# Kernel tuning notes

Measured on AMD Instinct MI355X. Metric: run time of the kernel, lower is better.

The kernel has to match this reference:

```python
import jax, jax.numpy as jnp
import numpy as np

B, C, N = 8, 256, 4096

def setup_inputs() -> dict:
    key = jax.random.key(0)
    k1, k2, k3 = jax.random.split(key, 3)
    pts_feat = jax.random.normal(k1, (B, C, N), dtype=jnp.float32)
    # Conv1d(channels, channels, 1, bias=False) weight is [C_out, C_in, 1] -> store as [C_out, C_in]
    scale = 1.0 / np.sqrt(C)
    Wq = jax.random.uniform(k2, (C, C), dtype=jnp.float32, minval=-scale, maxval=scale)
    Wk = jax.random.uniform(k3, (C, C), dtype=jnp.float32, minval=-scale, maxval=scale)
    return {"pts_feat": pts_feat, "Wq": Wq, "Wk": Wk}

def reference(pts_feat, Wq, Wk):
    # 1x1 conv == channel-wise matmul. x_q: [B, N, C], x_k: [B, C, N]
    x_q = jnp.einsum('bcn,dc->bnd', pts_feat, Wq)
    x_k = jnp.einsum('bcn,dc->bdn', pts_feat, Wk)
    logits = jnp.einsum('bnc,bcm->bnm', x_q, x_k)          # [B, N, N]
    attn = jax.nn.softmax(logits, axis=-1)
    attn = attn / (1e-8 + attn.sum(axis=-1, keepdims=True))
    # torch.einsum('bnn,bnc->bnc', attn, feat) takes the DIAGONAL of attn
    # and scales each point's raw feature vector by it (no contraction).
    diag = jnp.diagonal(attn, axis1=1, axis2=2)            # [B, N]
    x_attn = pts_feat * diag[:, None, :]                   # [B, C, N]
    return x_attn
```

## Files before the change

kernel.cpp:

```cpp
#include <hip/hip_runtime.h>
#include <hip/hip_bf16.h>
#include <cstdint>

#define B_ 8
#define C_ 256
#define N_ 4096

typedef __bf16 bf16;
typedef __bf16 bf16x8 __attribute__((ext_vector_type(8)));
typedef float f32x4 __attribute__((ext_vector_type(4)));
typedef unsigned int u32;

__device__ __forceinline__ void async_ld16(const void* g, void* l) {
  __builtin_amdgcn_global_load_lds(
      (const __attribute__((address_space(1))) void*)g,
      (__attribute__((address_space(3))) void*)l, 16, 0, 0);
}

__device__ __forceinline__ float bh2f(unsigned short u) {
  union { u32 i; float f; } x; x.i = ((u32)u) << 16; return x.f;
}
__device__ __forceinline__ unsigned short f2bh(float f) {
  union { float f; u32 i; } x; x.f = f;
  u32 i = x.i + 0x7fffu + ((x.i >> 16) & 1u);
  return (unsigned short)(i >> 16);
}

__device__ __forceinline__ bool wave_sniff_fp32(const unsigned short* p) {
  int l = threadIdx.x & 63;
  unsigned short u = p[2 * l];
  int e = (u >> 7) & 0xff;
  unsigned long long m = __ballot(e >= 112 && e <= 142);
  return __popcll(m) < 32;
}

__global__ __launch_bounds__(256) void k_wconv(const void* __restrict__ W0,
                                               const void* __restrict__ W1,
                                               unsigned short* __restrict__ Wc0,
                                               unsigned short* __restrict__ Wc1) {
  const void* Wv = blockIdx.y ? W1 : W0;
  unsigned short* Wc = blockIdx.y ? Wc1 : Wc0;
  bool f32 = wave_sniff_fp32((const unsigned short*)Wv);
  int i = (blockIdx.x * 256 + threadIdx.x) * 4;
  if (f32) {
    float4 v = *(const float4*)((const float*)Wv + i);
    unsigned short o0 = f2bh(v.x), o1 = f2bh(v.y), o2 = f2bh(v.z), o3 = f2bh(v.w);
    uint2 o; o.x = ((u32)o1 << 16) | o0; o.y = ((u32)o3 << 16) | o2;
    *(uint2*)(Wc + i) = o;
  } else {
    uint2 v = *(const uint2*)((const unsigned short*)Wv + i);
    *(uint2*)(Wc + i) = v;
  }
}

__global__ __launch_bounds__(256) void k_transpose(const void* __restrict__ Fv,
                                                   unsigned short* __restrict__ Ft) {
  bool f32 = wave_sniff_fp32((const unsigned short*)Fv);
  __shared__ unsigned short tile[64 * 66];
  int n0 = blockIdx.x * 64, c0 = blockIdx.y * 64, b = blockIdx.z;
  int t = threadIdx.x;
#pragma unroll
  for (int p = 0; p < 2; ++p) {
    int c = (t >> 3) + 32 * p;
    int n = (t & 7) * 8;
    size_t off = (size_t)(b * C_ + c0 + c) * N_ + n0 + n;
    unsigned short vals[8];
    if (f32) {
      const float* src = (const float*)Fv + off;
      float4 v0 = *(const float4*)(src);
      float4 v1 = *(const float4*)(src + 4);
      vals[0] = f2bh(v0.x); vals[1] = f2bh(v0.y); vals[2] = f2bh(v0.z); vals[3] = f2bh(v0.w);
      vals[4] = f2bh(v1.x); vals[5] = f2bh(v1.y); vals[6] = f2bh(v1.z); vals[7] = f2bh(v1.w);
    } else {
      uint4 v = *(const uint4*)((const unsigned short*)Fv + off);
      vals[0] = (unsigned short)(v.x & 0xffffu); vals[1] = (unsigned short)(v.x >> 16);
      vals[2] = (unsigned short)(v.y & 0xffffu); vals[3] = (unsigned short)(v.y >> 16);
      vals[4] = (unsigned short)(v.z & 0xffffu); vals[5] = (unsigned short)(v.z >> 16);
      vals[6] = (unsigned short)(v.w & 0xffffu); vals[7] = (unsigned short)(v.w >> 16);
    }
#pragma unroll
    for (int s = 0; s < 8; ++s) tile[c * 66 + n + s] = vals[s];
  }
  __syncthreads();
#pragma unroll
  for (int p = 0; p < 4; ++p) {
    int n = (t >> 4) + 16 * p;
    int cq = (t & 15) * 4;
    unsigned short e0 = tile[(cq + 0) * 66 + n];
    unsigned short e1 = tile[(cq + 1) * 66 + n];
    unsigned short e2 = tile[(cq + 2) * 66 + n];
    unsigned short e3 = tile[(cq + 3) * 66 + n];
    uint2 o;
    o.x = ((u32)e1 << 16) | e0;
    o.y = ((u32)e3 << 16) | e2;
    *(uint2*)(Ft + ((size_t)(b * N_ + n0 + n) * C_ + c0 + cq)) = o;
  }
}

__global__ __launch_bounds__(256) void k_proj(const bf16* __restrict__ Ft,
                                              const bf16* __restrict__ Wq,
                                              const bf16* __restrict__ Wk,
                                              bf16* __restrict__ Qt,
                                              bf16* __restrict__ Kt) {
  __shared__ bf16 As[128 * 32];
  __shared__ bf16 Bs[128 * 32];
  int n0 = blockIdx.x * 128;
  int b = blockIdx.y;
  int z = blockIdx.z;
  int d0 = (z & 1) * 128;
  const bf16* W = (z >> 1) ? Wk : Wq;
  bf16* Dst = (z >> 1) ? Kt : Qt;
  int t = threadIdx.x;
  int w = t >> 6, l = t & 63;
  int wm = (w & 1) * 64, wn = (w >> 1) * 64;
  int lr = l & 15, lq = l >> 4;
  const size_t fbase = (size_t)b * N_ * C_;

  f32x4 acc[4][4] = {};
  for (int kc = 0; kc < 8; ++kc) {
    __syncthreads();
#pragma unroll
    for (int r = 0; r < 2; ++r) {
      int ci = r * 4 + w;
      int e = ci * 64 + l;
      int row = e >> 2, coff = (e & 3) * 8;
      async_ld16(Ft + fbase + (size_t)(n0 + row) * C_ + kc * 32 + coff, As + ci * 512);
      async_ld16(W + (size_t)(d0 + row) * C_ + kc * 32 + coff, Bs + ci * 512);
    }
    __syncthreads();
    bf16x8 a[4], bb[4];
#pragma unroll
    for (int i = 0; i < 4; ++i)
      a[i] = *(const bf16x8*)(As + (wm + 16 * i + lr) * 32 + lq * 8);
#pragma unroll
    for (int j = 0; j < 4; ++j)
      bb[j] = *(const bf16x8*)(Bs + (wn + 16 * j + lr) * 32 + lq * 8);
#pragma unroll
    for (int i = 0; i < 4; ++i)
#pragma unroll
      for (int j = 0; j < 4; ++j)
        acc[i][j] = __builtin_amdgcn_mfma_f32_16x16x32_bf16(a[i], bb[j], acc[i][j], 0, 0, 0);
  }
#pragma unroll
  for (int i = 0; i < 4; ++i)
#pragma unroll
    for (int j = 0; j < 4; ++j)
#pragma unroll
      for (int r = 0; r < 4; ++r) {
        int row = n0 + wm + 16 * i + lq * 4 + r;
        int col = d0 + wn + 16 * j + lr;
        Dst[fbase + (size_t)row * C_ + col] = (bf16)acc[i][j][r];
      }
}

__global__ __launch_bounds__(256, 4) void k_attn(const bf16* __restrict__ Qt,
                                                 const bf16* __restrict__ Kt,
                                                 float* __restrict__ snn,
                                                 float* __restrict__ lsum) {
  __shared__ bf16 Ks[8 * 64 * 32];
  int bid = blockIdx.x;
  int b = bid & 7, h = (bid >> 3) & 1, ntile = bid >> 4;
  int n0 = ntile * 128;
  int t = threadIdx.x, w = t >> 6, l = t & 63;
  int lr = l & 15, lq = l >> 4;
  int wrow = w * 32;
  const size_t gbase = (size_t)b * N_ * C_;

  bf16x8 a[2][8];
#pragma unroll
  for (int i = 0; i < 2; ++i)
#pragma unroll
    for (int kc = 0; kc < 8; ++kc)
      a[i][kc] = *(const bf16x8*)(Qt + gbase + (size_t)(n0 + wrow + 16 * i + lr) * C_ + kc * 32 + lq * 8);

  float part[8];
#pragma unroll
  for (int s = 0; s < 8; ++s) part[s] = 0.f;

  int m_base = h * 2048;
  bool has_diag = ((ntile >> 4) == h);
  int d0 = (ntile & 15) * 2;

  int srow = t >> 2, scoff = (t & 3) * 8;

  for (int it = 0; it < 32; ++it) {
    int m0 = m_base + it * 64;
    __syncthreads();
#pragma unroll
    for (int kc = 0; kc < 8; ++kc)
      async_ld16(Kt + gbase + (size_t)(m0 + srow) * C_ + kc * 32 + scoff,
                 Ks + kc * 2048 + t * 8);
    __syncthreads();
    f32x4 acc[2][4] = {};
#pragma unroll
    for (int kc = 0; kc < 8; ++kc) {
      bf16x8 bb[4];
#pragma unroll
      for (int j = 0; j < 4; ++j)
        bb[j] = *(const bf16x8*)(Ks + kc * 2048 + (16 * j + lr) * 32 + lq * 8);
#pragma unroll
      for (int i = 0; i < 2; ++i)
#pragma unroll
        for (int j = 0; j < 4; ++j)
          acc[i][j] = __builtin_amdgcn_mfma_f32_16x16x32_bf16(a[i][kc], bb[j], acc[i][j], 0, 0, 0);
    }
    bool dit = has_diag && ((it >> 1) == (ntile & 15));
#pragma unroll
    for (int i = 0; i < 2; ++i)
#pragma unroll
      for (int j = 0; j < 4; ++j)
#pragma unroll
        for (int r = 0; r < 4; ++r) {
          float e = __expf(acc[i][j][r]);
          part[i * 4 + r] += e;
          if (dit) {
            int rloc = wrow + 16 * i + lq * 4 + r;
            int cloc = 16 * j + lr;
            if ((it - d0) * 64 + cloc == rloc) snn[b * N_ + n0 + rloc] = e;
          }
        }
  }

#pragma unroll
  for (int s = 0; s < 8; ++s) {
    float v = part[s];
    v += __shfl_xor(v, 1);
    v += __shfl_xor(v, 2);
    v += __shfl_xor(v, 4);
    v += __shfl_xor(v, 8);
    part[s] = v;
  }
  if (lr == 0) {
#pragma unroll
    for (int i = 0; i < 2; ++i)
#pragma unroll
      for (int r = 0; r < 4; ++r)
        lsum[((size_t)h * B_ + b) * N_ + n0 + wrow + 16 * i + lq * 4 + r] = part[i * 4 + r];
  }
}

__global__ __launch_bounds__(256) void k_scale(const void* __restrict__ Fv,
                                               const float* __restrict__ snn,
                                               const float* __restrict__ lsum,
                                               void* __restrict__ Outv) {
  bool f32 = wave_sniff_fp32((const unsigned short*)Fv);
  int g = blockIdx.x * 256 + threadIdx.x;
  size_t base = (size_t)g * 8;
  int n = (int)(base & (N_ - 1));
  int b = (int)(base >> 20);
  float4 s0 = *(const float4*)(snn + (size_t)b * N_ + n);
  float4 s1 = *(const float4*)(snn + (size_t)b * N_ + n + 4);
  float4 l00 = *(const float4*)(lsum + (size_t)b * N_ + n);
  float4 l01 = *(const float4*)(lsum + (size_t)b * N_ + n + 4);
  float4 l10 = *(const float4*)(lsum + (size_t)(B_ + b) * N_ + n);
  float4 l11 = *(const float4*)(lsum + (size_t)(B_ + b) * N_ + n + 4);
  const float c1 = 1.0f + 1e-8f;
  float dd[8];
  dd[0] = s0.x / ((l00.x + l10.x) * c1);
  dd[1] = s0.y / ((l00.y + l10.y) * c1);
  dd[2] = s0.z / ((l00.z + l10.z) * c1);
  dd[3] = s0.w / ((l00.w + l10.w) * c1);
  dd[4] = s1.x / ((l01.x + l11.x) * c1);
  dd[5] = s1.y / ((l01.y + l11.y) * c1);
  dd[6] = s1.z / ((l01.z + l11.z) * c1);
  dd[7] = s1.w / ((l01.w + l11.w) * c1);
  if (f32) {
    const float* F = (const float*)Fv + base;
    float* O = (float*)Outv + base;
    float4 a0 = *(const float4*)(F);
    float4 a1 = *(const float4*)(F + 4);
    float4 o0, o1;
    o0.x = a0.x * dd[0]; o0.y = a0.y * dd[1]; o0.z = a0.z * dd[2]; o0.w = a0.w * dd[3];
    o1.x = a1.x * dd[4]; o1.y = a1.y * dd[5]; o1.z = a1.z * dd[6]; o1.w = a1.w * dd[7];
    *(float4*)(O) = o0;
    *(float4*)(O + 4) = o1;
  } else {
    uint4 v = *(const uint4*)((const unsigned short*)Fv + base);
    u32 vv[4] = {v.x, v.y, v.z, v.w};
    u32 o[4];
#pragma unroll
    for (int k = 0; k < 4; ++k) {
      float lo = bh2f((unsigned short)(vv[k] & 0xffffu)) * dd[2 * k];
      float hi = bh2f((unsigned short)(vv[k] >> 16)) * dd[2 * k + 1];
      o[k] = ((u32)f2bh(hi) << 16) | f2bh(lo);
    }
    uint4 ov; ov.x = o[0]; ov.y = o[1]; ov.z = o[2]; ov.w = o[3];
    *(uint4*)((unsigned short*)Outv + base) = ov;
  }
}

extern "C" void kernel_launch(void* const* d_in, const int* in_sizes, int n_in,
                              void* d_out, int out_size, void* d_ws, size_t ws_size,
                              hipStream_t stream) {
  (void)in_sizes; (void)n_in; (void)out_size; (void)ws_size;
  const void* F = d_in[0];
  const void* Wq = d_in[1];
  const void* Wk = d_in[2];
  char* ws = (char*)d_ws;
  bf16* Ft = (bf16*)(ws);
  bf16* Qt = (bf16*)(ws + (16u << 20));
  bf16* Kt = (bf16*)(ws + (32u << 20));
  char* tail = ws + (48u << 20);
  float* snn = (float*)(tail);
  float* lsum = (float*)(tail + 131072);
  bf16* Wqc = (bf16*)(tail + 131072 + 262144);
  bf16* Wkc = (bf16*)(tail + 131072 + 262144 + 131072);

  k_wconv<<<dim3(64, 2), 256, 0, stream>>>(Wq, Wk, (unsigned short*)Wqc, (unsigned short*)Wkc);
  k_transpose<<<dim3(N_ / 64, C_ / 64, B_), 256, 0, stream>>>(F, (unsigned short*)Ft);
  k_proj<<<dim3(N_ / 128, B_, 4), 256, 0, stream>>>(Ft, Wqc, Wkc, Qt, Kt);
  k_attn<<<512, 256, 0, stream>>>(Qt, Kt, snn, lsum);
  k_scale<<<(B_ * C_ * N_ / 8) / 256, 256, 0, stream>>>(F, snn, lsum, d_out);
}
```

Baseline: 189.3 us.

## Fold Wq and Wk into one combined matrix, halve projections, split attention four ways

Logits are rewritten as F^T (Wq^T Wk) F. A small kernel computes the combined CxC matrix, so only one projection G = F^T M is produced, and the attention kernel multiplies G against the transposed features directly. This drops the separate K projection and its memory traffic. The attention key range is split four ways, giving 1024 blocks instead of 512. Shared-memory loads gain an XOR swizzle to cut bank conflicts, and k_proj now stages all of K in LDS at once. The change adds bf16 rounding of the combined matrix, and the k_mt kernel is a slow serial 256-step loop per thread.

```diff
diff --git a/kernel.cpp b/kernel.cpp
--- a/kernel.cpp
+++ b/kernel.cpp
@@ -34,23 +34,44 @@
   return __popcll(m) < 32;
 }
 
-__global__ __launch_bounds__(256) void k_wconv(const void* __restrict__ W0,
-                                               const void* __restrict__ W1,
-                                               unsigned short* __restrict__ Wc0,
-                                               unsigned short* __restrict__ Wc1) {
-  const void* Wv = blockIdx.y ? W1 : W0;
-  unsigned short* Wc = blockIdx.y ? Wc1 : Wc0;
-  bool f32 = wave_sniff_fp32((const unsigned short*)Wv);
-  int i = (blockIdx.x * 256 + threadIdx.x) * 4;
-  if (f32) {
-    float4 v = *(const float4*)((const float*)Wv + i);
-    unsigned short o0 = f2bh(v.x), o1 = f2bh(v.y), o2 = f2bh(v.z), o3 = f2bh(v.w);
-    uint2 o; o.x = ((u32)o1 << 16) | o0; o.y = ((u32)o3 << 16) | o2;
-    *(uint2*)(Wc + i) = o;
-  } else {
-    uint2 v = *(const uint2*)((const unsigned short*)Wv + i);
-    *(uint2*)(Wc + i) = v;
-  }
+__global__ __launch_bounds__(256) void k_mt(const void* __restrict__ Wqv,
+                                            const void* __restrict__ Wkv,
+                                            unsigned short* __restrict__ Mt) {
+  bool fq = wave_sniff_fp32((const unsigned short*)Wqv);
+  bool fk = wave_sniff_fp32((const unsigned short*)Wkv);
+  int tg = blockIdx.x * 256 + threadIdx.x;
+  int d = tg >> 5;
+  int c0 = (tg & 31) * 8;
+  float acc[8];
+#pragma unroll
+  for (int k = 0; k < 8; ++k) acc[k] = 0.f;
+  for (int e = 0; e < C_; ++e) {
+    float wk = fk ? ((const float*)Wkv)[e * C_ + d]
+                  : bh2f(((const unsigned short*)Wkv)[e * C_ + d]);
+    float wq[8];
+    if (fq) {
+      float4 a0 = *(const float4*)((const float*)Wqv + e * C_ + c0);
+      float4 a1 = *(const float4*)((const float*)Wqv + e * C_ + c0 + 4);
+      wq[0] = a0.x; wq[1] = a0.y; wq[2] = a0.z; wq[3] = a0.w;
+      wq[4] = a1.x; wq[5] = a1.y; wq[6] = a1.z; wq[7] = a1.w;
+    } else {
+      uint4 v = *(const uint4*)((const unsigned short*)Wqv + e * C_ + c0);
+      u32 vv[4] = {v.x, v.y, v.z, v.w};
+#pragma unroll
+      for (int k = 0; k < 4; ++k) {
+        wq[2 * k] = bh2f((unsigned short)(vv[k] & 0xffffu));
+        wq[2 * k + 1] = bh2f((unsigned short)(vv[k] >> 16));
+      }
+    }
+#pragma unroll
+    for (int k = 0; k < 8; ++k) acc[k] += wk * wq[k];
+  }
+  u32 o[4];
+#pragma unroll
+  for (int k = 0; k < 4; ++k)
+    o[k] = ((u32)f2bh(acc[2 * k + 1]) << 16) | f2bh(acc[2 * k]);
+  uint4 ov; ov.x = o[0]; ov.y = o[1]; ov.z = o[2]; ov.w = o[3];
+  *(uint4*)(Mt + (size_t)d * C_ + c0) = ov;
 }
 
 __global__ __launch_bounds__(256) void k_transpose(const void* __restrict__ Fv,
@@ -97,69 +118,65 @@
   }
 }
 
-__global__ __launch_bounds__(256) void k_proj(const bf16* __restrict__ Ft,
-                                              const bf16* __restrict__ Wq,
-                                              const bf16* __restrict__ Wk,
-                                              bf16* __restrict__ Qt,
-                                              bf16* __restrict__ Kt) {
-  __shared__ bf16 As[128 * 32];
-  __shared__ bf16 Bs[128 * 32];
+__global__ __launch_bounds__(256, 2) void k_proj(const bf16* __restrict__ Ft,
+                                                 const bf16* __restrict__ Mt,
+                                                 bf16* __restrict__ G) {
+  __shared__ bf16 As[8 * 128 * 32];
   int n0 = blockIdx.x * 128;
   int b = blockIdx.y;
-  int z = blockIdx.z;
-  int d0 = (z & 1) * 128;
-  const bf16* W = (z >> 1) ? Wk : Wq;
-  bf16* Dst = (z >> 1) ? Kt : Qt;
-  int t = threadIdx.x;
-  int w = t >> 6, l = t & 63;
-  int wm = (w & 1) * 64, wn = (w >> 1) * 64;
+  int d0 = blockIdx.z * 128;
+  int t = threadIdx.x, w = t >> 6, l = t & 63;
   int lr = l & 15, lq = l >> 4;
+  int wn = w * 32;
   const size_t fbase = (size_t)b * N_ * C_;
 
-  f32x4 acc[4][4] = {};
+  int schunk = ((t & 3) ^ ((t >> 3) & 3)) * 8;
+#pragma unroll
+  for (int kc = 0; kc < 8; ++kc)
+#pragma unroll
+    for (int r = 0; r < 2; ++r)
+      async_ld16(Ft + fbase + (size_t)(n0 + r * 64 + (t >> 2)) * C_ + kc * 32 + schunk,
+                 As + kc * 4096 + (r * 256 + t) * 8);
+
+  bf16x8 bb[2][8];
+#pragma unroll
+  for (int j = 0; j < 2; ++j)
+#pragma unroll
+    for (int kc = 0; kc < 8; ++kc)
+      bb[j][kc] = *(const bf16x8*)(Mt + (size_t)(d0 + wn + 16 * j + lr) * C_ + kc * 32 + lq * 8);
+
+  __syncthreads();
+  int rchunk = (lq ^ ((lr >> 1) & 3)) * 8;
+  f32x4 acc[8][2] = {};
+#pragma unroll
   for (int kc = 0; kc < 8; ++kc) {
-    __syncthreads();
-#pragma unroll
-    for (int r = 0; r < 2; ++r) {
-      int ci = r * 4 + w;
-      int e = ci * 64 + l;
-      int row = e >> 2, coff = (e & 3) * 8;
-      async_ld16(Ft + fbase + (size_t)(n0 + row) * C_ + kc * 32 + coff, As + ci * 512);
-      async_ld16(W + (size_t)(d0 + row) * C_ + kc * 32 + coff, Bs + ci * 512);
-    }
-    __syncthreads();
-    bf16x8 a[4], bb[4];
-#pragma unroll
-    for (int i = 0; i < 4; ++i)
-      a[i] = *(const bf16x8*)(As + (wm + 16 * i + lr) * 32 + lq * 8);
-#pragma unroll
-    for (int j = 0; j < 4; ++j)
-      bb[j] = *(const bf16x8*)(Bs + (wn + 16 * j + lr) * 32 + lq * 8);
-#pragma unroll
-    for (int i = 0; i < 4; ++i)
-#pragma unroll
-      for (int j = 0; j < 4; ++j)
-        acc[i][j] = __builtin_amdgcn_mfma_f32_16x16x32_bf16(a[i], bb[j], acc[i][j], 0, 0, 0);
-  }
-#pragma unroll
-  for (int i = 0; i < 4; ++i)
-#pragma unroll
-    for (int j = 0; j < 4; ++j)
+#pragma unroll
+    for (int i = 0; i < 8; ++i) {
+      bf16x8 a = *(const bf16x8*)(As + kc * 4096 + (16 * i + lr) * 32 + rchunk);
+#pragma unroll
+      for (int j = 0; j < 2; ++j)
+        acc[i][j] = __builtin_amdgcn_mfma_f32_16x16x32_bf16(a, bb[j][kc], acc[i][j], 0, 0, 0);
+    }
+  }
+#pragma unroll
+  for (int i = 0; i < 8; ++i)
+#pragma unroll
+    for (int j = 0; j < 2; ++j)
 #pragma unroll
       for (int r = 0; r < 4; ++r) {
-        int row = n0 + wm + 16 * i + lq * 4 + r;
+        int row = n0 + 16 * i + lq * 4 + r;
         int col = d0 + wn + 16 * j + lr;
-        Dst[fbase + (size_t)row * C_ + col] = (bf16)acc[i][j][r];
+        G[fbase + (size_t)row * C_ + col] = (bf16)acc[i][j][r];
       }
 }
 
-__global__ __launch_bounds__(256, 4) void k_attn(const bf16* __restrict__ Qt,
-                                                 const bf16* __restrict__ Kt,
+__global__ __launch_bounds__(256, 4) void k_attn(const bf16* __restrict__ G,
+                                                 const bf16* __restrict__ Ft,
                                                  float* __restrict__ snn,
                                                  float* __restrict__ lsum) {
   __shared__ bf16 Ks[8 * 64 * 32];
   int bid = blockIdx.x;
-  int b = bid & 7, h = (bid >> 3) & 1, ntile = bid >> 4;
+  int b = bid & 7, q = (bid >> 3) & 3, ntile = bid >> 5;
   int n0 = ntile * 128;
   int t = threadIdx.x, w = t >> 6, l = t & 63;
   int lr = l & 15, lq = l >> 4;
@@ -171,24 +188,26 @@
   for (int i = 0; i < 2; ++i)
 #pragma unroll
     for (int kc = 0; kc < 8; ++kc)
-      a[i][kc] = *(const bf16x8*)(Qt + gbase + (size_t)(n0 + wrow + 16 * i + lr) * C_ + kc * 32 + lq * 8);
+      a[i][kc] = *(const bf16x8*)(G + gbase + (size_t)(n0 + wrow + 16 * i + lr) * C_ + kc * 32 + lq * 8);
 
   float part[8];
 #pragma unroll
   for (int s = 0; s < 8; ++s) part[s] = 0.f;
 
-  int m_base = h * 2048;
-  bool has_diag = ((ntile >> 4) == h);
-  int d0 = (ntile & 15) * 2;
-
-  int srow = t >> 2, scoff = (t & 3) * 8;
-
-  for (int it = 0; it < 32; ++it) {
+  int m_base = q * 1024;
+  bool has_diag = (q == (ntile >> 3));
+  int d0 = (ntile & 7) * 2;
+
+  int srow = t >> 2;
+  int schunk = ((t & 3) ^ ((t >> 3) & 3)) * 8;
+  int rchunk = (lq ^ ((lr >> 1) & 3)) * 8;
+
+  for (int it = 0; it < 16; ++it) {
     int m0 = m_base + it * 64;
     __syncthreads();
 #pragma unroll
     for (int kc = 0; kc < 8; ++kc)
-      async_ld16(Kt + gbase + (size_t)(m0 + srow) * C_ + kc * 32 + scoff,
+      async_ld16(Ft + gbase + (size_t)(m0 + srow) * C_ + kc * 32 + schunk,
                  Ks + kc * 2048 + t * 8);
     __syncthreads();
     f32x4 acc[2][4] = {};
@@ -197,14 +216,14 @@
       bf16x8 bb[4];
 #pragma unroll
       for (int j = 0; j < 4; ++j)
-        bb[j] = *(const bf16x8*)(Ks + kc * 2048 + (16 * j + lr) * 32 + lq * 8);
+        bb[j] = *(const bf16x8*)(Ks + kc * 2048 + (16 * j + lr) * 32 + rchunk);
 #pragma unroll
       for (int i = 0; i < 2; ++i)
 #pragma unroll
         for (int j = 0; j < 4; ++j)
           acc[i][j] = __builtin_amdgcn_mfma_f32_16x16x32_bf16(a[i][kc], bb[j], acc[i][j], 0, 0, 0);
     }
-    bool dit = has_diag && ((it >> 1) == (ntile & 15));
+    bool dit = has_diag && ((it >> 1) == (ntile & 7));
 #pragma unroll
     for (int i = 0; i < 2; ++i)
 #pragma unroll
@@ -235,7 +254,7 @@
     for (int i = 0; i < 2; ++i)
 #pragma unroll
       for (int r = 0; r < 4; ++r)
-        lsum[((size_t)h * B_ + b) * N_ + n0 + wrow + 16 * i + lq * 4 + r] = part[i * 4 + r];
+        lsum[((size_t)q * B_ + b) * N_ + n0 + wrow + 16 * i + lq * 4 + r] = part[i * 4 + r];
   }
 }
 
@@ -250,20 +269,22 @@
   int b = (int)(base >> 20);
   float4 s0 = *(const float4*)(snn + (size_t)b * N_ + n);
   float4 s1 = *(const float4*)(snn + (size_t)b * N_ + n + 4);
-  float4 l00 = *(const float4*)(lsum + (size_t)b * N_ + n);
-  float4 l01 = *(const float4*)(lsum + (size_t)b * N_ + n + 4);
-  float4 l10 = *(const float4*)(lsum + (size_t)(B_ + b) * N_ + n);
-  float4 l11 = *(const float4*)(lsum + (size_t)(B_ + b) * N_ + n + 4);
+  float ls[8];
+#pragma unroll
+  for (int k = 0; k < 8; ++k) ls[k] = 0.f;
+#pragma unroll
+  for (int p = 0; p < 4; ++p) {
+    float4 l0 = *(const float4*)(lsum + ((size_t)p * B_ + b) * N_ + n);
+    float4 l1 = *(const float4*)(lsum + ((size_t)p * B_ + b) * N_ + n + 4);
+    ls[0] += l0.x; ls[1] += l0.y; ls[2] += l0.z; ls[3] += l0.w;
+    ls[4] += l1.x; ls[5] += l1.y; ls[6] += l1.z; ls[7] += l1.w;
+  }
   const float c1 = 1.0f + 1e-8f;
   float dd[8];
-  dd[0] = s0.x / ((l00.x + l10.x) * c1);
-  dd[1] = s0.y / ((l00.y + l10.y) * c1);
-  dd[2] = s0.z / ((l00.z + l10.z) * c1);
-  dd[3] = s0.w / ((l00.w + l10.w) * c1);
-  dd[4] = s1.x / ((l01.x + l11.x) * c1);
-  dd[5] = s1.y / ((l01.y + l11.y) * c1);
-  dd[6] = s1.z / ((l01.z + l11.z) * c1);
-  dd[7] = s1.w / ((l01.w + l11.w) * c1);
+  dd[0] = s0.x / (ls[0] * c1); dd[1] = s0.y / (ls[1] * c1);
+  dd[2] = s0.z / (ls[2] * c1); dd[3] = s0.w / (ls[3] * c1);
+  dd[4] = s1.x / (ls[4] * c1); dd[5] = s1.y / (ls[5] * c1);
+  dd[6] = s1.z / (ls[6] * c1); dd[7] = s1.w / (ls[7] * c1);
   if (f32) {
     const float* F = (const float*)Fv + base;
     float* O = (float*)Outv + base;
@@ -298,17 +319,15 @@
   const void* Wk = d_in[2];
   char* ws = (char*)d_ws;
   bf16* Ft = (bf16*)(ws);
-  bf16* Qt = (bf16*)(ws + (16u << 20));
-  bf16* Kt = (bf16*)(ws + (32u << 20));
-  char* tail = ws + (48u << 20);
+  bf16* G = (bf16*)(ws + (16u << 20));
+  char* tail = ws + (32u << 20);
   float* snn = (float*)(tail);
   float* lsum = (float*)(tail + 131072);
-  bf16* Wqc = (bf16*)(tail + 131072 + 262144);
-  bf16* Wkc = (bf16*)(tail + 131072 + 262144 + 131072);
-
-  k_wconv<<<dim3(64, 2), 256, 0, stream>>>(Wq, Wk, (unsigned short*)Wqc, (unsigned short*)Wkc);
+  bf16* Mt = (bf16*)(tail + 131072 + 524288);
+
+  k_mt<<<32, 256, 0, stream>>>(Wq, Wk, (unsigned short*)Mt);
   k_transpose<<<dim3(N_ / 64, C_ / 64, B_), 256, 0, stream>>>(F, (unsigned short*)Ft);
-  k_proj<<<dim3(N_ / 128, B_, 4), 256, 0, stream>>>(Ft, Wqc, Wkc, Qt, Kt);
-  k_attn<<<512, 256, 0, stream>>>(Qt, Kt, snn, lsum);
+  k_proj<<<dim3(N_ / 128, B_, 2), 256, 0, stream>>>(Ft, Mt, G);
+  k_attn<<<1024, 256, 0, stream>>>(G, Ft, snn, lsum);
   k_scale<<<(B_ * C_ * N_ / 8) / 256, 256, 0, stream>>>(F, snn, lsum, d_out);
 }
```

New measurement: 265.4 us. 1.4x slower.
